# Kernel tuning notes

Hardware: AMD Instinct MI355X
Metric: run time of the kernel (lower is better)

## Reference

```python
import jax, jax.numpy as jnp
import numpy as np

N, E = 50000, 800000
IN, HID, HEADS, OUT = 128, 16, 4, 40
NEG_SLOPE = 0.2
BN_EPS = 1e-5


def gat_conv(x, edge_src, edge_dst, W, a_src, a_dst, b, heads, out_ch, concat):
    """PyG GATConv: linear -> per-head attention logits -> segment softmax over
    incoming edges of each target node -> weighted scatter-sum. Self-loops are
    assumed already appended to edge_src/edge_dst."""
    n = x.shape[0]
    h = (x @ W.T).reshape(n, heads, out_ch)              # [N, H, C]
    alpha_s = jnp.sum(h * a_src, axis=-1)                # [N, H]
    alpha_d = jnp.sum(h * a_dst, axis=-1)                # [N, H]
    logits = jax.nn.leaky_relu(alpha_s[edge_src] + alpha_d[edge_dst], NEG_SLOPE)  # [E', H]
    # numerically-stable segment softmax over edges grouped by target node
    seg_max = jax.ops.segment_max(logits, edge_dst, num_segments=n)
    e = jnp.exp(logits - seg_max[edge_dst])
    seg_sum = jax.ops.segment_sum(e, edge_dst, num_segments=n)
    alpha = e / (seg_sum[edge_dst] + 1e-16)              # [E', H]
    msg = h[edge_src] * alpha[:, :, None]                # [E', H, C]
    out = jax.ops.segment_sum(msg, edge_dst, num_segments=n)  # [N, H, C]
    out = out.reshape(n, heads * out_ch) if concat else out.mean(axis=1)
    return out + b


def batch_norm(x, gamma, beta):
    mean = x.mean(axis=0)
    var = x.var(axis=0)  # biased, matching torch BN normalization
    return (x - mean) * jax.lax.rsqrt(var + BN_EPS) * gamma + beta


def setup_inputs() -> dict:
    key = jax.random.key(0)
    ks = jax.random.split(key, 16)
    H = HID * HEADS  # 64
    inp = {
        "x": jax.random.normal(ks[0], (N, IN), jnp.float32),
        "edge_index": jax.random.randint(ks[1], (2, E), 0, N, jnp.int64),
        # layer 0: IN -> HID, HEADS heads, concat
        "W0": jax.random.normal(ks[2], (H, IN), jnp.float32) * 0.05,
        "a_src0": jax.random.normal(ks[3], (1, HEADS, HID), jnp.float32) * 0.05,
        "a_dst0": jax.random.normal(ks[4], (1, HEADS, HID), jnp.float32) * 0.05,
        "b0": jnp.zeros((H,), jnp.float32),
        # layer 1: H -> HID, HEADS heads, concat
        "W1": jax.random.normal(ks[5], (H, H), jnp.float32) * 0.05,
        "a_src1": jax.random.normal(ks[6], (1, HEADS, HID), jnp.float32) * 0.05,
        "a_dst1": jax.random.normal(ks[7], (1, HEADS, HID), jnp.float32) * 0.05,
        "b1": jnp.zeros((H,), jnp.float32),
        # layer 2: H -> OUT, 1 head, concat=False
        "W2": jax.random.normal(ks[8], (OUT, H), jnp.float32) * 0.05,
        "a_src2": jax.random.normal(ks[9], (1, 1, OUT), jnp.float32) * 0.05,
        "a_dst2": jax.random.normal(ks[10], (1, 1, OUT), jnp.float32) * 0.05,
        "b2": jnp.zeros((OUT,), jnp.float32),
        # batchnorms
        "g0": jnp.ones((H,), jnp.float32), "bt0": jnp.zeros((H,), jnp.float32),
        "g1": jnp.ones((H,), jnp.float32), "bt1": jnp.zeros((H,), jnp.float32),
    }
    return inp


def reference(x, edge_index, W0, a_src0, a_dst0, b0, W1, a_src1, a_dst1, b1,
              W2, a_src2, a_dst2, b2, g0, bt0, g1, bt1):
    n = x.shape[0]
    loop = jnp.arange(n, dtype=edge_index.dtype)
    src = jnp.concatenate([edge_index[0], loop])  # PyG add_self_loops=True
    dst = jnp.concatenate([edge_index[1], loop])

    h = gat_conv(x, src, dst, W0, a_src0, a_dst0, b0, HEADS, HID, True)
    h = batch_norm(h, g0, bt0)
    h = gat_conv(h, src, dst, W1, a_src1, a_dst1, b1, HEADS, HID, True)
    h = batch_norm(h, g1, bt1)
    emb = gat_conv(h, src, dst, W2, a_src2, a_dst2, b2, 1, OUT, False)
    return jax.nn.log_softmax(emb, axis=1), emb
```

## Files before the change

kernel.cpp:

```cpp
#include <hip/hip_runtime.h>
#include <hip/hip_bf16.h>
#include <math.h>

#define NN 50000
#define NE 800000
#define CURPAD 16
#define CAP 64

using short8 = __attribute__((ext_vector_type(8))) short;
using f32x4  = __attribute__((ext_vector_type(4))) float;

__device__ inline short bfbits(float f) {
    __hip_bfloat16 b = __float2bfloat16(f);
    return __builtin_bit_cast(short, b);
}
__device__ inline short8 cvt8(float4 lo, float4 hi) {
    short8 r;
    r[0] = bfbits(lo.x); r[1] = bfbits(lo.y); r[2] = bfbits(lo.z); r[3] = bfbits(lo.w);
    r[4] = bfbits(hi.x); r[5] = bfbits(hi.y); r[6] = bfbits(hi.z); r[7] = bfbits(hi.w);
    return r;
}

template<int K, int CT, int COUT, int HEADSN, bool FUSESCAT>
__global__ __launch_bounds__(256) void mfma_gemm(
    const float* __restrict__ x, const float* __restrict__ W,
    const float* __restrict__ a_src, const float* __restrict__ a_dst,
    const float* __restrict__ bnsc, const float* __restrict__ bnsh,
    ushort* __restrict__ h, float* __restrict__ as_out, float* __restrict__ ad_out,
    int n, int scat_blocks,
    const int* __restrict__ esrc, const int* __restrict__ edst,
    int* __restrict__ cnt, unsigned* __restrict__ pk2)
{
    if (FUSESCAT && (int)blockIdx.x < scat_blocks) {
        int base = ((int)blockIdx.x * 256 + (int)threadIdx.x) * 8;
        int d[8], sv[8], pv[8];
#pragma unroll
        for (int j = 0; j < 8; j++) {
            d[j] = (base + j < NE) ? edst[base + j] : -1;
            sv[j] = (base + j < NE) ? esrc[base + j] : 0;
        }
#pragma unroll
        for (int j = 0; j < 8; j++)
            pv[j] = (d[j] >= 0) ? atomicAdd(&cnt[(size_t)d[j] * CURPAD], 1) : 0;
#pragma unroll
        for (int j = 0; j < 8; j++)
            if (d[j] >= 0 && pv[j] < CAP)
                pk2[((size_t)d[j] << 6) + pv[j]] = (unsigned)sv[j];
        return;
    }

    int bid = (int)blockIdx.x - (FUSESCAT ? scat_blocks : 0);
    int tid = threadIdx.x;
    int w = tid >> 6, l = tid & 63;
    int l15 = l & 15, g = l >> 4;
    int m_base = bid * 64 + w * 16;

    f32x4 acc[CT];
#pragma unroll
    for (int ct = 0; ct < CT; ct++) acc[ct] = f32x4{0.f, 0.f, 0.f, 0.f};

    int arow = m_base + l15; if (arow >= n) arow = n - 1;
    const float* xrow = x + (size_t)arow * K;

#pragma unroll
    for (int ks = 0; ks < K / 32; ks++) {
        int k0 = ks * 32 + g * 8;
        float4 lo = *(const float4*)(xrow + k0);
        float4 hi = *(const float4*)(xrow + k0 + 4);
        if (bnsc) {
            float4 s0 = *(const float4*)(bnsc + k0), s1 = *(const float4*)(bnsc + k0 + 4);
            float4 t0 = *(const float4*)(bnsh + k0), t1 = *(const float4*)(bnsh + k0 + 4);
            lo.x = lo.x * s0.x + t0.x; lo.y = lo.y * s0.y + t0.y;
            lo.z = lo.z * s0.z + t0.z; lo.w = lo.w * s0.w + t0.w;
            hi.x = hi.x * s1.x + t1.x; hi.y = hi.y * s1.y + t1.y;
            hi.z = hi.z * s1.z + t1.z; hi.w = hi.w * s1.w + t1.w;
        }
        short8 a = cvt8(lo, hi);
#pragma unroll
        for (int ct = 0; ct < CT; ct++) {
            int wrow = ct * 16 + l15;
            if (wrow >= COUT) wrow = COUT - 1;
            const float* Wr = W + (size_t)wrow * K;
            float4 blo = *(const float4*)(Wr + k0);
            float4 bhi = *(const float4*)(Wr + k0 + 4);
            short8 b = cvt8(blo, bhi);
            acc[ct] = __builtin_amdgcn_mfma_f32_16x16x32_bf16(a, b, acc[ct], 0, 0, 0);
        }
    }

#pragma unroll
    for (int ct = 0; ct < CT; ct++) {
#pragma unroll
        for (int r = 0; r < 4; r++) {
            int row = m_base + g * 4 + r;
            int col = ct * 16 + l15;
            if (row < n && col < COUT)
                h[(size_t)row * COUT + col] = (ushort)bfbits(acc[ct][r]);
        }
    }

    if (HEADSN == 4) {
        float asv[CT], adv[CT];
#pragma unroll
        for (int ct = 0; ct < CT; ct++) {
            asv[ct] = a_src[ct * 16 + l15];
            adv[ct] = a_dst[ct * 16 + l15];
        }
#pragma unroll
        for (int r = 0; r < 4; r++) {
            float rs[CT], rd[CT];
#pragma unroll
            for (int ct = 0; ct < CT; ct++) {
                rs[ct] = acc[ct][r] * asv[ct];
                rd[ct] = acc[ct][r] * adv[ct];
            }
#pragma unroll
            for (int off = 1; off < 16; off <<= 1) {
#pragma unroll
                for (int ct = 0; ct < CT; ct++) {
                    rs[ct] += __shfl_xor(rs[ct], off);
                    rd[ct] += __shfl_xor(rd[ct], off);
                }
            }
            int row = m_base + g * 4 + r;
            if (row < n) {
#pragma unroll
                for (int ct = 0; ct < CT; ct++) {
                    if (l15 == ct) {
                        as_out[row * 4 + ct] = rs[ct];
                        ad_out[row * 4 + ct] = rd[ct];
                    }
                }
            }
        }
    } else {
        float asv[CT], adv[CT];
#pragma unroll
        for (int ct = 0; ct < CT; ct++) {
            int col = ct * 16 + l15;
            asv[ct] = (col < COUT) ? a_src[col] : 0.f;
            adv[ct] = (col < COUT) ? a_dst[col] : 0.f;
        }
#pragma unroll
        for (int r = 0; r < 4; r++) {
            float rs = 0.f, rd = 0.f;
#pragma unroll
            for (int ct = 0; ct < CT; ct++) {
                rs += acc[ct][r] * asv[ct];
                rd += acc[ct][r] * adv[ct];
            }
#pragma unroll
            for (int off = 1; off < 16; off <<= 1) {
                rs += __shfl_xor(rs, off);
                rd += __shfl_xor(rd, off);
            }
            int row = m_base + g * 4 + r;
            if (row < n && l15 == 0) {
                as_out[row] = rs;
                ad_out[row] = rd;
            }
        }
    }
}

template<int CH, int HEADSN, bool LSM, bool BNP>
__global__ __launch_bounds__(256) void gat_kernel(
    const ushort* __restrict__ h, const float* __restrict__ as,
    const float* __restrict__ ad, const int* __restrict__ cnt,
    const unsigned* __restrict__ pk2, const float* __restrict__ bias,
    float* __restrict__ out, float* __restrict__ psum, float* __restrict__ psq,
    int n)
{
    __shared__ float lsv[4][64];
    int tid = threadIdx.x;
    int w = tid >> 6;
    int wid = blockIdx.x * 4 + w;
    int lane = tid & 63;
    int sub = lane & 7, eslot = lane >> 3;
    int c0 = sub * 8;
    bool act = (c0 < CH);
    int hd = (HEADSN == 1) ? 0 : (sub >> 1);
    float adi = ad[wid * HEADSN + hd];

    float ac0 = 0.f, ac1 = 0.f, ac2 = 0.f, ac3 = 0.f;
    float ac4 = 0.f, ac5 = 0.f, ac6 = 0.f, ac7 = 0.f;
    float ss = 0.f;

    int deg = cnt[(size_t)wid * CURPAD];
    if (deg > CAP) deg = CAP;
    int slotbase = wid << 6;
    int nit = (deg + 7) >> 3;
    int pos = eslot;
    bool ok = pos < deg;
    int s = 0; float av = 0.f;
    if (ok) { s = (int)pk2[slotbase + pos]; av = as[s * HEADSN + hd]; }
    for (int it = 0; it < nit; ++it) {
        int posn = pos + 8;
        bool ok2 = (it + 1 < nit) && (posn < deg);
        int s2 = 0; float av2 = 0.f;
        if (ok2) { s2 = (int)pk2[slotbase + posn]; av2 = as[s2 * HEADSN + hd]; }
        float p = 0.f;
        if (ok) {
            float lg = av + adi;
            lg = (lg > 0.f) ? lg : 0.2f * lg;
            p = __expf(fminf(lg, 60.f));
        }
        float h0 = 0.f, h1 = 0.f, h2 = 0.f, h3 = 0.f, h4 = 0.f, h5 = 0.f, h6 = 0.f, h7 = 0.f;
        if (act) {
            uint4 u = *(const uint4*)&h[(size_t)s * CH + c0];
            h0 = __uint_as_float((u.x & 0xffffu) << 16);
            h1 = __uint_as_float(u.x & 0xffff0000u);
            h2 = __uint_as_float((u.y & 0xffffu) << 16);
            h3 = __uint_as_float(u.y & 0xffff0000u);
            h4 = __uint_as_float((u.z & 0xffffu) << 16);
            h5 = __uint_as_float(u.z & 0xffff0000u);
            h6 = __uint_as_float((u.w & 0xffffu) << 16);
            h7 = __uint_as_float(u.w & 0xffff0000u);
        }
        ss += p;
        ac0 += p * h0;  ac1 += p * h1;  ac2 += p * h2;  ac3 += p * h3;
        ac4 += p * h4;  ac5 += p * h5;  ac6 += p * h6;  ac7 += p * h7;
        s = s2; av = av2; ok = ok2; pos = posn;
    }

#pragma unroll
    for (int o = 8; o <= 32; o <<= 1) {
        ss  += __shfl_xor(ss, o);
        ac0 += __shfl_xor(ac0, o);  ac1 += __shfl_xor(ac1, o);
        ac2 += __shfl_xor(ac2, o);  ac3 += __shfl_xor(ac3, o);
        ac4 += __shfl_xor(ac4, o);  ac5 += __shfl_xor(ac5, o);
        ac6 += __shfl_xor(ac6, o);  ac7 += __shfl_xor(ac7, o);
    }

    {
        float lg = as[wid * HEADSN + hd] + adi;
        lg = (lg > 0.f) ? lg : 0.2f * lg;
        float ps = __expf(fminf(lg, 60.f));
        ss += ps;
        if (act) {
            uint4 u = *(const uint4*)&h[(size_t)wid * CH + c0];
            ac0 += ps * __uint_as_float((u.x & 0xffffu) << 16);
            ac1 += ps * __uint_as_float(u.x & 0xffff0000u);
            ac2 += ps * __uint_as_float((u.y & 0xffffu) << 16);
            ac3 += ps * __uint_as_float(u.y & 0xffff0000u);
            ac4 += ps * __uint_as_float((u.z & 0xffffu) << 16);
            ac5 += ps * __uint_as_float(u.z & 0xffff0000u);
            ac6 += ps * __uint_as_float((u.w & 0xffffu) << 16);
            ac7 += ps * __uint_as_float(u.w & 0xffff0000u);
        }
    }

    float inv = 1.f / (ss + 1e-16f);
    float4 bv0 = make_float4(0.f, 0.f, 0.f, 0.f), bv1 = bv0;
    if (act) {
        bv0 = *(const float4*)&bias[c0];
        bv1 = *(const float4*)&bias[c0 + 4];
    }
    float v0 = ac0 * inv + bv0.x;
    float v1 = ac1 * inv + bv0.y;
    float v2 = ac2 * inv + bv0.z;
    float v3 = ac3 * inv + bv0.w;
    float v4 = ac4 * inv + bv1.x;
    float v5 = ac5 * inv + bv1.y;
    float v6 = ac6 * inv + bv1.z;
    float v7 = ac7 * inv + bv1.w;

    if (BNP) {
        if (eslot == 0) {
            lsv[w][c0 + 0] = v0; lsv[w][c0 + 1] = v1;
            lsv[w][c0 + 2] = v2; lsv[w][c0 + 3] = v3;
            lsv[w][c0 + 4] = v4; lsv[w][c0 + 5] = v5;
            lsv[w][c0 + 6] = v6; lsv[w][c0 + 7] = v7;
        }
        __syncthreads();
        if (tid < 64) {
            float a0 = lsv[0][tid], a1 = lsv[1][tid], a2 = lsv[2][tid], a3 = lsv[3][tid];
            psum[(size_t)blockIdx.x * 64 + tid] = (a0 + a1) + (a2 + a3);
            psq[(size_t)blockIdx.x * 64 + tid]  = (a0 * a0 + a1 * a1) + (a2 * a2 + a3 * a3);
        }
    }

    if (LSM) {
        float mx = act ? fmaxf(fmaxf(fmaxf(v0, v1), fmaxf(v2, v3)),
                               fmaxf(fmaxf(v4, v5), fmaxf(v6, v7))) : -INFINITY;
        for (int o = 4; o >= 1; o >>= 1) mx = fmaxf(mx, __shfl_xor(mx, o));
        float sse = 0.f;
        if (act)
            sse = __expf(v0 - mx) + __expf(v1 - mx) + __expf(v2 - mx) + __expf(v3 - mx)
                + __expf(v4 - mx) + __expf(v5 - mx) + __expf(v6 - mx) + __expf(v7 - mx);
        for (int o = 4; o >= 1; o >>= 1) sse += __shfl_xor(sse, o);
        float ls = logf(sse);
        if (eslot == 0 && act) {
            *(float4*)&out[(size_t)wid * CH + c0] =
                make_float4(v0 - mx - ls, v1 - mx - ls, v2 - mx - ls, v3 - mx - ls);
            *(float4*)&out[(size_t)wid * CH + c0 + 4] =
                make_float4(v4 - mx - ls, v5 - mx - ls, v6 - mx - ls, v7 - mx - ls);
            *(float4*)&out[(size_t)n * CH + (size_t)wid * CH + c0] =
                make_float4(v0, v1, v2, v3);
            *(float4*)&out[(size_t)n * CH + (size_t)wid * CH + c0 + 4] =
                make_float4(v4, v5, v6, v7);
        }
    } else {
        if (eslot == 0 && act) {
            *(float4*)&out[(size_t)wid * CH + c0] = make_float4(v0, v1, v2, v3);
            *(float4*)&out[(size_t)wid * CH + c0 + 4] = make_float4(v4, v5, v6, v7);
        }
    }
}

__global__ __launch_bounds__(256) void bn_reduce(
    const float* __restrict__ psum, const float* __restrict__ psq,
    const float* __restrict__ g, const float* __restrict__ bt,
    float* __restrict__ sc, float* __restrict__ sh, int nb, int n)
{
    int c = blockIdx.x;
    int t = threadIdx.x;
    float s = 0.f, s2 = 0.f;
    for (int r = t; r < nb; r += 256) {
        s  += psum[(size_t)r * 64 + c];
        s2 += psq[(size_t)r * 64 + c];
    }
    __shared__ float a[256], b[256];
    a[t] = s; b[t] = s2; __syncthreads();
    for (int o = 128; o >= 1; o >>= 1) {
        if (t < o) { a[t] += a[t + o]; b[t] += b[t + o]; }
        __syncthreads();
    }
    if (t == 0) {
        float mean = a[0] / n;
        float var = b[0] / n - mean * mean;
        float invs = rsqrtf(var + 1e-5f);
        float scale = g[c] * invs;
        sc[c] = scale;
        sh[c] = bt[c] - mean * scale;
    }
}

extern "C" void kernel_launch(void* const* d_in, const int* in_sizes, int n_in,
                              void* d_out, int out_size, void* d_ws, size_t ws_size,
                              hipStream_t stream) {
    const float* x   = (const float*)d_in[0];
    const int*   ei  = (const int*)d_in[1];
    const float* W0  = (const float*)d_in[2];
    const float* as0 = (const float*)d_in[3];
    const float* ad0 = (const float*)d_in[4];
    const float* b0  = (const float*)d_in[5];
    const float* W1  = (const float*)d_in[6];
    const float* as1 = (const float*)d_in[7];
    const float* ad1 = (const float*)d_in[8];
    const float* b1  = (const float*)d_in[9];
    const float* W2  = (const float*)d_in[10];
    const float* as2 = (const float*)d_in[11];
    const float* ad2 = (const float*)d_in[12];
    const float* b2  = (const float*)d_in[13];
    const float* g0  = (const float*)d_in[14];
    const float* bt0 = (const float*)d_in[15];
    const float* g1  = (const float*)d_in[16];
    const float* bt1 = (const float*)d_in[17];

    const int* esrc = ei;
    const int* edst = ei + NE;

    char* ws = (char*)d_ws;
    size_t off = 0;
    auto alloc = [&](size_t bytes) {
        void* p = ws + off;
        off += (bytes + 255) & ~(size_t)255;
        return p;
    };
    int* cnt      = (int*)alloc((size_t)NN * CURPAD * 4);
    unsigned* pk2 = (unsigned*)alloc((size_t)NN * CAP * 4);
    ushort* hbuf  = (ushort*)alloc((size_t)NN * 64 * 2);
    float* obuf   = (float*)alloc((size_t)NN * 64 * 4);
    float* asb    = (float*)alloc((size_t)NN * 4 * 4);
    float* adb    = (float*)alloc((size_t)NN * 4 * 4);
    float* psum   = (float*)alloc((size_t)(NN / 4) * 64 * 4);
    float* psq    = (float*)alloc((size_t)(NN / 4) * 64 * 4);
    float* sc     = (float*)alloc(64 * 4);
    float* sh     = (float*)alloc(64 * 4);

    const int SCB = (NE + 2047) / 2048;
    const int GBM = (NN + 63) / 64;
    const int GB4 = NN / 4;

    hipMemsetAsync(cnt, 0, (size_t)NN * CURPAD * 4, stream);
    mfma_gemm<128, 4, 64, 4, true><<<SCB + GBM, 256, 0, stream>>>(
        x, W0, as0, ad0, nullptr, nullptr, hbuf, asb, adb, NN, SCB,
        esrc, edst, cnt, pk2);

    gat_kernel<64, 4, false, true><<<GB4, 256, 0, stream>>>(
        hbuf, asb, adb, cnt, pk2, b0, obuf, psum, psq, NN);
    bn_reduce<<<64, 256, 0, stream>>>(psum, psq, g0, bt0, sc, sh, GB4, NN);

    mfma_gemm<64, 4, 64, 4, false><<<GBM, 256, 0, stream>>>(
        obuf, W1, as1, ad1, sc, sh, hbuf, asb, adb, NN, 0,
        nullptr, nullptr, nullptr, nullptr);
    gat_kernel<64, 4, false, true><<<GB4, 256, 0, stream>>>(
        hbuf, asb, adb, cnt, pk2, b1, obuf, psum, psq, NN);
    bn_reduce<<<64, 256, 0, stream>>>(psum, psq, g1, bt1, sc, sh, GB4, NN);

    mfma_gemm<64, 3, 40, 1, false><<<GBM, 256, 0, stream>>>(
        obuf, W2, as2, ad2, sc, sh, hbuf, asb, adb, NN, 0,
        nullptr, nullptr, nullptr, nullptr);
    gat_kernel<40, 1, true, false><<<GB4, 256, 0, stream>>>(
        hbuf, asb, adb, cnt, pk2, b2, (float*)d_out, nullptr, nullptr, NN);
}
```

Before: 252.8 us.

## Store intermediate activations in bf16, fold batchnorm into weights, deepen gather prefetch

The GAT aggregation kernel now writes its hidden outputs as bf16 instead of fp32, halving the intermediate activation traffic read by the next GEMM. The batchnorm affine is folded into the next layer's weights and a per-column bias by a small bn_fold kernel, so the GEMM reads pre-converted bf16 weights and skips the per-element scale and shift. The edge gather loop is restructured to prefetch two edges ahead, including the neighbour feature row, to hide gather latency. In exchange, the BN-normalised inputs are quantised to bf16 one step earlier (before rather than after normalisation), and each of the two folds adds a single-block kernel launch.

```diff
diff --git a/kernel.cpp b/kernel.cpp
--- a/kernel.cpp
+++ b/kernel.cpp
@@ -21,11 +21,11 @@
     return r;
 }
 
-template<int K, int CT, int COUT, int HEADSN, bool FUSESCAT>
+template<int K, int CT, int COUT, int HEADSN, bool FUSESCAT, bool BF16IN>
 __global__ __launch_bounds__(256) void mfma_gemm(
-    const float* __restrict__ x, const float* __restrict__ W,
+    const void* __restrict__ xv, const void* __restrict__ Wv,
+    const float* __restrict__ cb,
     const float* __restrict__ a_src, const float* __restrict__ a_dst,
-    const float* __restrict__ bnsc, const float* __restrict__ bnsh,
     ushort* __restrict__ h, float* __restrict__ as_out, float* __restrict__ ad_out,
     int n, int scat_blocks,
     const int* __restrict__ esrc, const int* __restrict__ edst,
@@ -60,32 +60,43 @@
     for (int ct = 0; ct < CT; ct++) acc[ct] = f32x4{0.f, 0.f, 0.f, 0.f};
 
     int arow = m_base + l15; if (arow >= n) arow = n - 1;
-    const float* xrow = x + (size_t)arow * K;
 
 #pragma unroll
     for (int ks = 0; ks < K / 32; ks++) {
         int k0 = ks * 32 + g * 8;
-        float4 lo = *(const float4*)(xrow + k0);
-        float4 hi = *(const float4*)(xrow + k0 + 4);
-        if (bnsc) {
-            float4 s0 = *(const float4*)(bnsc + k0), s1 = *(const float4*)(bnsc + k0 + 4);
-            float4 t0 = *(const float4*)(bnsh + k0), t1 = *(const float4*)(bnsh + k0 + 4);
-            lo.x = lo.x * s0.x + t0.x; lo.y = lo.y * s0.y + t0.y;
-            lo.z = lo.z * s0.z + t0.z; lo.w = lo.w * s0.w + t0.w;
-            hi.x = hi.x * s1.x + t1.x; hi.y = hi.y * s1.y + t1.y;
-            hi.z = hi.z * s1.z + t1.z; hi.w = hi.w * s1.w + t1.w;
-        }
-        short8 a = cvt8(lo, hi);
+        short8 a;
+        if (BF16IN) {
+            const ushort* xrow = (const ushort*)xv + (size_t)arow * K;
+            a = *(const short8*)(xrow + k0);
+        } else {
+            const float* xrow = (const float*)xv + (size_t)arow * K;
+            float4 lo = *(const float4*)(xrow + k0);
+            float4 hi = *(const float4*)(xrow + k0 + 4);
+            a = cvt8(lo, hi);
+        }
 #pragma unroll
         for (int ct = 0; ct < CT; ct++) {
             int wrow = ct * 16 + l15;
             if (wrow >= COUT) wrow = COUT - 1;
-            const float* Wr = W + (size_t)wrow * K;
-            float4 blo = *(const float4*)(Wr + k0);
-            float4 bhi = *(const float4*)(Wr + k0 + 4);
-            short8 b = cvt8(blo, bhi);
+            short8 b;
+            if (BF16IN) {
+                const ushort* Wr = (const ushort*)Wv + (size_t)wrow * K;
+                b = *(const short8*)(Wr + k0);
+            } else {
+                const float* Wr = (const float*)Wv + (size_t)wrow * K;
+                float4 blo = *(const float4*)(Wr + k0);
+                float4 bhi = *(const float4*)(Wr + k0 + 4);
+                b = cvt8(blo, bhi);
+            }
             acc[ct] = __builtin_amdgcn_mfma_f32_16x16x32_bf16(a, b, acc[ct], 0, 0, 0);
         }
+    }
+
+    float cbv[CT];
+#pragma unroll
+    for (int ct = 0; ct < CT; ct++) {
+        int col = ct * 16 + l15;
+        cbv[ct] = (BF16IN && cb) ? cb[(col < COUT) ? col : (COUT - 1)] : 0.f;
     }
 
 #pragma unroll
@@ -95,7 +106,7 @@
             int row = m_base + g * 4 + r;
             int col = ct * 16 + l15;
             if (row < n && col < COUT)
-                h[(size_t)row * COUT + col] = (ushort)bfbits(acc[ct][r]);
+                h[(size_t)row * COUT + col] = (ushort)bfbits(acc[ct][r] + cbv[ct]);
         }
     }
 
@@ -111,8 +122,9 @@
             float rs[CT], rd[CT];
 #pragma unroll
             for (int ct = 0; ct < CT; ct++) {
-                rs[ct] = acc[ct][r] * asv[ct];
-                rd[ct] = acc[ct][r] * adv[ct];
+                float hv = acc[ct][r] + cbv[ct];
+                rs[ct] = hv * asv[ct];
+                rd[ct] = hv * adv[ct];
             }
 #pragma unroll
             for (int off = 1; off < 16; off <<= 1) {
@@ -146,8 +158,9 @@
             float rs = 0.f, rd = 0.f;
 #pragma unroll
             for (int ct = 0; ct < CT; ct++) {
-                rs += acc[ct][r] * asv[ct];
-                rd += acc[ct][r] * adv[ct];
+                float hv = acc[ct][r] + cbv[ct];
+                rs += hv * asv[ct];
+                rd += hv * adv[ct];
             }
 #pragma unroll
             for (int off = 1; off < 16; off <<= 1) {
@@ -168,8 +181,8 @@
     const ushort* __restrict__ h, const float* __restrict__ as,
     const float* __restrict__ ad, const int* __restrict__ cnt,
     const unsigned* __restrict__ pk2, const float* __restrict__ bias,
-    float* __restrict__ out, float* __restrict__ psum, float* __restrict__ psq,
-    int n)
+    float* __restrict__ outf, ushort* __restrict__ outb,
+    float* __restrict__ psum, float* __restrict__ psq, int n)
 {
     __shared__ float lsv[4][64];
     int tid = threadIdx.x;
@@ -191,36 +204,43 @@
     int slotbase = wid << 6;
     int nit = (deg + 7) >> 3;
     int pos = eslot;
-    bool ok = pos < deg;
-    int s = 0; float av = 0.f;
-    if (ok) { s = (int)pk2[slotbase + pos]; av = as[s * HEADSN + hd]; }
+
+    bool ok0 = pos < deg;
+    int s0 = 0; float av0 = 0.f;
+    if (ok0) { s0 = (int)pk2[slotbase + pos]; av0 = as[s0 * HEADSN + hd]; }
+    bool ok1 = (pos + 8) < deg;
+    int s1 = 0; float av1 = 0.f;
+    if (ok1) { s1 = (int)pk2[slotbase + pos + 8]; av1 = as[s1 * HEADSN + hd]; }
+    uint4 h0 = make_uint4(0, 0, 0, 0);
+    if (ok0 && act) h0 = *(const uint4*)&h[(size_t)s0 * CH + c0];
+
     for (int it = 0; it < nit; ++it) {
-        int posn = pos + 8;
-        bool ok2 = (it + 1 < nit) && (posn < deg);
+        int pos2 = pos + 16;
+        bool ok2 = pos2 < deg;
         int s2 = 0; float av2 = 0.f;
-        if (ok2) { s2 = (int)pk2[slotbase + posn]; av2 = as[s2 * HEADSN + hd]; }
+        if (ok2) { s2 = (int)pk2[slotbase + pos2]; av2 = as[s2 * HEADSN + hd]; }
+        uint4 h1 = make_uint4(0, 0, 0, 0);
+        if (ok1 && act) h1 = *(const uint4*)&h[(size_t)s1 * CH + c0];
+
         float p = 0.f;
-        if (ok) {
-            float lg = av + adi;
+        if (ok0) {
+            float lg = av0 + adi;
             lg = (lg > 0.f) ? lg : 0.2f * lg;
             p = __expf(fminf(lg, 60.f));
         }
-        float h0 = 0.f, h1 = 0.f, h2 = 0.f, h3 = 0.f, h4 = 0.f, h5 = 0.f, h6 = 0.f, h7 = 0.f;
-        if (act) {
-            uint4 u = *(const uint4*)&h[(size_t)s * CH + c0];
-            h0 = __uint_as_float((u.x & 0xffffu) << 16);
-            h1 = __uint_as_float(u.x & 0xffff0000u);
-            h2 = __uint_as_float((u.y & 0xffffu) << 16);
-            h3 = __uint_as_float(u.y & 0xffff0000u);
-            h4 = __uint_as_float((u.z & 0xffffu) << 16);
-            h5 = __uint_as_float(u.z & 0xffff0000u);
-            h6 = __uint_as_float((u.w & 0xffffu) << 16);
-            h7 = __uint_as_float(u.w & 0xffff0000u);
-        }
         ss += p;
-        ac0 += p * h0;  ac1 += p * h1;  ac2 += p * h2;  ac3 += p * h3;
-        ac4 += p * h4;  ac5 += p * h5;  ac6 += p * h6;  ac7 += p * h7;
-        s = s2; av = av2; ok = ok2; pos = posn;
+        ac0 += p * __uint_as_float(h0.x << 16);
+        ac1 += p * __uint_as_float(h0.x & 0xffff0000u);
+        ac2 += p * __uint_as_float(h0.y << 16);
+        ac3 += p * __uint_as_float(h0.y & 0xffff0000u);
+        ac4 += p * __uint_as_float(h0.z << 16);
+        ac5 += p * __uint_as_float(h0.z & 0xffff0000u);
+        ac6 += p * __uint_as_float(h0.w << 16);
+        ac7 += p * __uint_as_float(h0.w & 0xffff0000u);
+
+        s0 = s1; av0 = av1; ok0 = ok1;
+        s1 = s2; av1 = av2; ok1 = ok2;
+        h0 = h1; pos += 8;
     }
 
 #pragma unroll
@@ -239,13 +259,13 @@
         ss += ps;
         if (act) {
             uint4 u = *(const uint4*)&h[(size_t)wid * CH + c0];
-            ac0 += ps * __uint_as_float((u.x & 0xffffu) << 16);
+            ac0 += ps * __uint_as_float(u.x << 16);
             ac1 += ps * __uint_as_float(u.x & 0xffff0000u);
-            ac2 += ps * __uint_as_float((u.y & 0xffffu) << 16);
+            ac2 += ps * __uint_as_float(u.y << 16);
             ac3 += ps * __uint_as_float(u.y & 0xffff0000u);
-            ac4 += ps * __uint_as_float((u.z & 0xffffu) << 16);
+            ac4 += ps * __uint_as_float(u.z << 16);
             ac5 += ps * __uint_as_float(u.z & 0xffff0000u);
-            ac6 += ps * __uint_as_float((u.w & 0xffffu) << 16);
+            ac6 += ps * __uint_as_float(u.w << 16);
             ac7 += ps * __uint_as_float(u.w & 0xffff0000u);
         }
     }
@@ -291,19 +311,21 @@
         for (int o = 4; o >= 1; o >>= 1) sse += __shfl_xor(sse, o);
         float ls = logf(sse);
         if (eslot == 0 && act) {
-            *(float4*)&out[(size_t)wid * CH + c0] =
+            *(float4*)&outf[(size_t)wid * CH + c0] =
                 make_float4(v0 - mx - ls, v1 - mx - ls, v2 - mx - ls, v3 - mx - ls);
-            *(float4*)&out[(size_t)wid * CH + c0 + 4] =
+            *(float4*)&outf[(size_t)wid * CH + c0 + 4] =
                 make_float4(v4 - mx - ls, v5 - mx - ls, v6 - mx - ls, v7 - mx - ls);
-            *(float4*)&out[(size_t)n * CH + (size_t)wid * CH + c0] =
+            *(float4*)&outf[(size_t)n * CH + (size_t)wid * CH + c0] =
                 make_float4(v0, v1, v2, v3);
-            *(float4*)&out[(size_t)n * CH + (size_t)wid * CH + c0 + 4] =
+            *(float4*)&outf[(size_t)n * CH + (size_t)wid * CH + c0 + 4] =
                 make_float4(v4, v5, v6, v7);
         }
     } else {
         if (eslot == 0 && act) {
-            *(float4*)&out[(size_t)wid * CH + c0] = make_float4(v0, v1, v2, v3);
-            *(float4*)&out[(size_t)wid * CH + c0 + 4] = make_float4(v4, v5, v6, v7);
+            short8 r;
+            r[0] = bfbits(v0); r[1] = bfbits(v1); r[2] = bfbits(v2); r[3] = bfbits(v3);
+            r[4] = bfbits(v4); r[5] = bfbits(v5); r[6] = bfbits(v6); r[7] = bfbits(v7);
+            *(short8*)&outb[(size_t)wid * CH + c0] = r;
         }
     }
 }
@@ -333,6 +355,23 @@
         float scale = g[c] * invs;
         sc[c] = scale;
         sh[c] = bt[c] - mean * scale;
+    }
+}
+
+__global__ __launch_bounds__(256) void bn_fold(
+    const float* __restrict__ sc, const float* __restrict__ sh,
+    const float* __restrict__ W, ushort* __restrict__ Wb,
+    float* __restrict__ cb, int cout, int k)
+{
+    int t = threadIdx.x;
+    for (int idx = t; idx < cout * k; idx += 256) {
+        int kk = idx % k;
+        Wb[idx] = (ushort)bfbits(W[idx] * sc[kk]);
+    }
+    if (t < cout) {
+        float s = 0.f;
+        for (int kk = 0; kk < k; kk++) s += sh[kk] * W[t * k + kk];
+        cb[t] = s;
     }
 }
 
@@ -371,37 +410,43 @@
     int* cnt      = (int*)alloc((size_t)NN * CURPAD * 4);
     unsigned* pk2 = (unsigned*)alloc((size_t)NN * CAP * 4);
     ushort* hbuf  = (ushort*)alloc((size_t)NN * 64 * 2);
-    float* obuf   = (float*)alloc((size_t)NN * 64 * 4);
+    ushort* obuf  = (ushort*)alloc((size_t)NN * 64 * 2);
     float* asb    = (float*)alloc((size_t)NN * 4 * 4);
     float* adb    = (float*)alloc((size_t)NN * 4 * 4);
     float* psum   = (float*)alloc((size_t)(NN / 4) * 64 * 4);
     float* psq    = (float*)alloc((size_t)(NN / 4) * 64 * 4);
     float* sc     = (float*)alloc(64 * 4);
     float* sh     = (float*)alloc(64 * 4);
+    ushort* W1b   = (ushort*)alloc(64 * 64 * 2);
+    ushort* W2b   = (ushort*)alloc(40 * 64 * 2);
+    float* cb1    = (float*)alloc(64 * 4);
+    float* cb2    = (float*)alloc(40 * 4);
 
     const int SCB = (NE + 2047) / 2048;
     const int GBM = (NN + 63) / 64;
     const int GB4 = NN / 4;
 
     hipMemsetAsync(cnt, 0, (size_t)NN * CURPAD * 4, stream);
-    mfma_gemm<128, 4, 64, 4, true><<<SCB + GBM, 256, 0, stream>>>(
-        x, W0, as0, ad0, nullptr, nullptr, hbuf, asb, adb, NN, SCB,
+    mfma_gemm<128, 4, 64, 4, true, false><<<SCB + GBM, 256, 0, stream>>>(
+        x, W0, nullptr, as0, ad0, hbuf, asb, adb, NN, SCB,
         esrc, edst, cnt, pk2);
 
     gat_kernel<64, 4, false, true><<<GB4, 256, 0, stream>>>(
-        hbuf, asb, adb, cnt, pk2, b0, obuf, psum, psq, NN);
+        hbuf, asb, adb, cnt, pk2, b0, nullptr, obuf, psum, psq, NN);
     bn_reduce<<<64, 256, 0, stream>>>(psum, psq, g0, bt0, sc, sh, GB4, NN);
-
-    mfma_gemm<64, 4, 64, 4, false><<<GBM, 256, 0, stream>>>(
-        obuf, W1, as1, ad1, sc, sh, hbuf, asb, adb, NN, 0,
+    bn_fold<<<1, 256, 0, stream>>>(sc, sh, W1, W1b, cb1, 64, 64);
+
+    mfma_gemm<64, 4, 64, 4, false, true><<<GBM, 256, 0, stream>>>(
+        obuf, W1b, cb1, as1, ad1, hbuf, asb, adb, NN, 0,
         nullptr, nullptr, nullptr, nullptr);
     gat_kernel<64, 4, false, true><<<GB4, 256, 0, stream>>>(
-        hbuf, asb, adb, cnt, pk2, b1, obuf, psum, psq, NN);
+        hbuf, asb, adb, cnt, pk2, b1, nullptr, obuf, psum, psq, NN);
     bn_reduce<<<64, 256, 0, stream>>>(psum, psq, g1, bt1, sc, sh, GB4, NN);
-
-    mfma_gemm<64, 3, 40, 1, false><<<GBM, 256, 0, stream>>>(
-        obuf, W2, as2, ad2, sc, sh, hbuf, asb, adb, NN, 0,
+    bn_fold<<<1, 256, 0, stream>>>(sc, sh, W2, W2b, cb2, 40, 64);
+
+    mfma_gemm<64, 3, 40, 1, false, true><<<GBM, 256, 0, stream>>>(
+        obuf, W2b, cb2, as2, ad2, hbuf, asb, adb, NN, 0,
         nullptr, nullptr, nullptr, nullptr);
     gat_kernel<40, 1, true, false><<<GB4, 256, 0, stream>>>(
-        hbuf, asb, adb, cnt, pk2, b2, (float*)d_out, nullptr, nullptr, NN);
-}
+        hbuf, asb, adb, cnt, pk2, b2, (float*)d_out, nullptr, nullptr, nullptr, NN);
+}
```

Measured after the change: 252.9 us. No clear change (+0.1%).
